# Optimization experiments

Hardware: AMD Instinct MI355X
Metric: run time of the kernel (lower is better)

The kernel has to match this reference:

```python
import jax, jax.numpy as jnp
import numpy as np

ITERS = 10
LAM = 0.1
EPS = 1e-5
DN = ('NCHW', 'OIHW', 'NCHW')


def conv2d(x, w, b, pad, dil=1):
    y = jax.lax.conv_general_dilated(
        x, w, window_strides=(1, 1), padding=((pad, pad), (pad, pad)),
        rhs_dilation=(dil, dil), dimension_numbers=DN)
    return y + b[None, :, None, None]


def avg_pool3(x):
    # F.avg_pool2d(k=3, s=1, p=1, count_include_pad=True): zero-pad then /9
    k = jnp.ones((1, 1, 3, 3), x.dtype) / 9.0
    return jax.lax.conv_general_dilated(
        x, k, window_strides=(1, 1), padding=((1, 1), (1, 1)), dimension_numbers=DN)


def setup_inputs() -> dict:
    key = jax.random.key(0)
    ks = jax.random.split(key, 16)
    B, H, W = 8, 512, 512
    G = 8  # guidance_channels
    s = 0.1
    return {
        'x': jax.random.normal(ks[0], (B, 1, H, W), jnp.float32),
        'gw1': jax.random.normal(ks[1], (16, 1, 3, 3), jnp.float32) * s,
        'gb1': jax.random.normal(ks[2], (16,), jnp.float32) * s,
        'bn_gamma': jax.random.normal(ks[3], (16,), jnp.float32) * s + 1.0,
        'bn_beta': jax.random.normal(ks[4], (16,), jnp.float32) * s,
        'bn_mean': jax.random.normal(ks[5], (16,), jnp.float32) * s,
        'bn_var': jax.random.uniform(ks[6], (16,), jnp.float32, 0.5, 1.5),
        'gw2': jax.random.normal(ks[7], (G, 16, 3, 3), jnp.float32) * s,
        'gb2': jax.random.normal(ks[8], (G,), jnp.float32) * s,
        'cw1': jax.random.normal(ks[9], (32, 4 + G, 3, 3), jnp.float32) * s,
        'cb1': jax.random.normal(ks[10], (32,), jnp.float32) * s,
        'cw2': jax.random.normal(ks[11], (16, 32, 3, 3), jnp.float32) * s,
        'cb2': jax.random.normal(ks[12], (16,), jnp.float32) * s,
        'cw3': jax.random.normal(ks[13], (4, 16, 3, 3), jnp.float32) * s,
        'cb3': jax.random.normal(ks[14], (4,), jnp.float32) * s,
    }


def reference(x, gw1, gb1, bn_gamma, bn_beta, bn_mean, bn_var, gw2, gb2,
              cw1, cb1, cw2, cb2, cw3, cb3):
    # guidance encoder on smoothed input (BN in eval mode with running stats)
    xs = avg_pool3(x)
    g = conv2d(xs, gw1, gb1, pad=2, dil=2)
    inv = bn_gamma / jnp.sqrt(bn_var + EPS)
    g = g * inv[None, :, None, None] + (bn_beta - bn_mean * inv)[None, :, None, None]
    g = jax.nn.relu(g)
    guidance = jax.lax.stop_gradient(jax.nn.sigmoid(conv2d(g, gw2, gb2, pad=1)))

    def step(x, _):
        xp = jnp.pad(x, ((0, 0), (0, 0), (1, 1), (1, 1)), mode='edge')
        gN = xp[:, :, :-2, 1:-1] - x
        gS = xp[:, :, 2:, 1:-1] - x
        gE = xp[:, :, 1:-1, 2:] - x
        gW = xp[:, :, 1:-1, :-2] - x
        comb = jnp.concatenate([gN, gS, gE, gW, guidance], axis=1)
        c = jax.nn.relu(conv2d(comb, cw1, cb1, pad=1))
        c = jax.nn.relu(conv2d(c, cw2, cb2, pad=1))
        c = jax.nn.sigmoid(conv2d(c, cw3, cb3, pad=1))
        cN, cS, cE, cWd = c[:, 0:1], c[:, 1:2], c[:, 2:3], c[:, 3:4]
        x = x + LAM * (cN * gN + cS * gS + cE * gE + cWd * gW)
        return x, None

    x, _ = jax.lax.scan(step, x, None, length=ITERS)
    return x
```

## Files before the change

### kernel.cpp

```cpp
#include <hip/hip_runtime.h>
#include <hip/hip_bf16.h>

#define HH 512
#define WW 512
#define NB 8
#define TT 16
#define BSG 384
#define BSI 256
#define EPSV 1e-5f
#define LAMV 0.1f

typedef __attribute__((ext_vector_type(4))) float f32x4;
typedef __attribute__((ext_vector_type(4))) short s16x4;
typedef __attribute__((ext_vector_type(8))) short s16x8;

#define MFMA16 __builtin_amdgcn_mfma_f32_16x16x32_bf16

#define W2PK 0
#define W3PK 9216
#define W1PKG 10816
#define W1PKU 14912
#define WPKTOT 21056

__device__ __forceinline__ float sigmoidf_(float v) { return 1.0f / (1.0f + __expf(-v)); }

__device__ __forceinline__ short f2bf(float f) {
    __hip_bfloat16 h = __float2bfloat16(f);
    short s; __builtin_memcpy(&s, &h, 2); return s;
}
__device__ __forceinline__ unsigned pack2bf(float a, float b) {
    __hip_bfloat16 ha = __float2bfloat16(a), hb = __float2bfloat16(b);
    unsigned short ua, ub;
    __builtin_memcpy(&ua, &ha, 2); __builtin_memcpy(&ub, &hb, 2);
    return (unsigned)ua | ((unsigned)ub << 16);
}

__global__ __launch_bounds__(256) void prep_kernel(
    const float* __restrict__ cw1, const float* __restrict__ cw2,
    const float* __restrict__ cw3, unsigned short* __restrict__ wpk)
{
    const int tid = threadIdx.x;
    for (int e = tid; e < 4608; e += 256) {
        int ch = e & 31, co = (e >> 5) & 15, t = e >> 9;
        wpk[W2PK / 2 + e] = (unsigned short)f2bf(cw2[(co * 32 + ch) * 9 + t]);
    }
    for (int e = tid; e < 800; e += 256) {
        int k = e % 160, row = e / 160;
        float v = 0.f;
        if (row < 4 && k < 144) { int tp = k / 16, ci = k & 15; v = cw3[(row * 16 + ci) * 9 + tp]; }
        wpk[W3PK / 2 + e] = (unsigned short)f2bf(v);
    }
    for (int e = tid; e < 2048; e += 256) {
        int k = e & 63, co = e >> 6;
        float v = 0.f;
        if (k < 36) { int tp = k >> 2, ch = k & 3; v = cw1[(co * 12 + ch) * 9 + tp]; }
        wpk[W1PKG / 2 + e] = (unsigned short)f2bf(v);
    }
    for (int e = tid; e < 3072; e += 256) {
        int k = e % 96, co = e / 96;
        float v = 0.f;
        if (k < 72) { int tp = k >> 3, ch = k & 7; v = cw1[(co * 12 + 4 + ch) * 9 + tp]; }
        wpk[W1PKU / 2 + e] = (unsigned short)f2bf(v);
    }
}

__global__ __launch_bounds__(BSG) void guidance_kernel(
    const float* __restrict__ x, const float* __restrict__ gw1, const float* __restrict__ gb1,
    const float* __restrict__ bng, const float* __restrict__ bnb, const float* __restrict__ bnm,
    const float* __restrict__ bnv, const float* __restrict__ gw2, const float* __restrict__ gb2,
    unsigned short* __restrict__ guid16)
{
    __shared__ __align__(16) float s_wg1[9][16];
    __shared__ __align__(16) float s_wg2[16][9][8];
    __shared__ float s_inv[16], s_off[16], s_b1[16], s_b2[8];
    __shared__ float s_x[24][25];
    __shared__ float s_xs[22][23];
    __shared__ float s_g[16][18][19];

    const int tid = threadIdx.x;
    const int b  = blockIdx.z;
    const int i0 = blockIdx.y * TT, j0 = blockIdx.x * TT;
    const int o = i0 - 4, p = j0 - 4;
    const float* xb = x + (size_t)b * HH * WW;

    for (int e = tid; e < 144; e += BSG) { int co = e % 16, t = e / 16; s_wg1[t][co] = gw1[co * 9 + t]; }
    for (int e = tid; e < 1152; e += BSG) {
        int co = e % 8, t = (e / 8) % 9, ci = e / 72;
        s_wg2[ci][t][co] = gw2[(co * 16 + ci) * 9 + t];
    }
    if (tid < 16) {
        float iv = bng[tid] * rsqrtf(bnv[tid] + EPSV);
        s_inv[tid] = iv; s_off[tid] = bnb[tid] - bnm[tid] * iv; s_b1[tid] = gb1[tid];
    }
    if (tid < 8) s_b2[tid] = gb2[tid];

    for (int e = tid; e < 576; e += BSG) {
        int r = e / 24, c = e % 24;
        int gi = o + r, gj = p + c;
        float v = 0.f;
        if (gi >= 0 && gi < HH && gj >= 0 && gj < WW) v = xb[gi * WW + gj];
        s_x[r][c] = v;
    }
    __syncthreads();

    for (int e = tid; e < 484; e += BSG) {
        int a = e / 22, bb = e % 22;
        int gi = o + a + 1, gj = p + bb + 1;
        float v = 0.f;
        if (gi >= 0 && gi < HH && gj >= 0 && gj < WW) {
            float s = 0.f;
            #pragma unroll
            for (int dr = 0; dr < 3; ++dr)
                #pragma unroll
                for (int dc = 0; dc < 3; ++dc) s += s_x[a + dr][bb + dc];
            v = s * (1.0f / 9.0f);
        }
        s_xs[a][bb] = v;
    }
    __syncthreads();

    for (int e = tid; e < 324; e += BSG) {
        int a = e / 18, bb = e % 18;
        int gi = o + a + 3, gj = p + bb + 3;
        bool in = (gi >= 0 && gi < HH && gj >= 0 && gj < WW);
        float acc[16];
        #pragma unroll
        for (int k = 0; k < 16; ++k) acc[k] = s_b1[k];
        #pragma unroll
        for (int kh = 0; kh < 3; ++kh)
            #pragma unroll
            for (int kw = 0; kw < 3; ++kw) {
                float av = s_xs[a + 2 * kh][bb + 2 * kw];
                #pragma unroll
                for (int q4 = 0; q4 < 4; ++q4) {
                    const float4 w = *(const float4*)&s_wg1[kh * 3 + kw][q4 * 4];
                    acc[q4*4+0] = fmaf(w.x, av, acc[q4*4+0]);
                    acc[q4*4+1] = fmaf(w.y, av, acc[q4*4+1]);
                    acc[q4*4+2] = fmaf(w.z, av, acc[q4*4+2]);
                    acc[q4*4+3] = fmaf(w.w, av, acc[q4*4+3]);
                }
            }
        #pragma unroll
        for (int k = 0; k < 16; ++k) {
            float val = acc[k] * s_inv[k] + s_off[k];
            s_g[k][a][bb] = in ? fmaxf(val, 0.f) : 0.f;
        }
    }
    __syncthreads();

    if (tid < 256) {
        int a = tid / 16, bb = tid % 16;
        int gi = i0 + a, gj = j0 + bb;
        float acc[8];
        #pragma unroll
        for (int k = 0; k < 8; ++k) acc[k] = s_b2[k];
        for (int ci = 0; ci < 16; ++ci)
            #pragma unroll
            for (int t9 = 0; t9 < 9; ++t9) {
                float av = s_g[ci][a + t9 / 3][bb + t9 % 3];
                #pragma unroll
                for (int q4 = 0; q4 < 2; ++q4) {
                    const float4 w = *(const float4*)&s_wg2[ci][t9][q4 * 4];
                    acc[q4*4+0] = fmaf(w.x, av, acc[q4*4+0]);
                    acc[q4*4+1] = fmaf(w.y, av, acc[q4*4+1]);
                    acc[q4*4+2] = fmaf(w.z, av, acc[q4*4+2]);
                    acc[q4*4+3] = fmaf(w.w, av, acc[q4*4+3]);
                }
            }
        uint4 u;
        u.x = pack2bf(sigmoidf_(acc[0]), sigmoidf_(acc[1]));
        u.y = pack2bf(sigmoidf_(acc[2]), sigmoidf_(acc[3]));
        u.z = pack2bf(sigmoidf_(acc[4]), sigmoidf_(acc[5]));
        u.w = pack2bf(sigmoidf_(acc[6]), sigmoidf_(acc[7]));
        *(uint4*)&guid16[(((size_t)b * HH + gi) * WW + gj) * 8] = u;
    }
}

__global__ __launch_bounds__(BSI) void iter_kernel(
    const float* __restrict__ xin, float* __restrict__ xout,
    const unsigned short* __restrict__ guid16,
    const unsigned short* __restrict__ wpk, const float* __restrict__ cb1,
    const float* __restrict__ cb2, const float* __restrict__ cb3)
{
    constexpr int ACTG = 2304;
    constexpr int ACTU = 6176;
    constexpr int C1   = 13920;
    constexpr int C2   = 40800;
    constexpr int C3   = C1;
    constexpr int TOT  = 51744;
    constexpr int C1P  = 6720;
    constexpr int C2P  = 5472;

    __shared__ __align__(16) char S[TOT];
    float* s_x = (float*)S;

    const int tid = threadIdx.x;
    const int bz = blockIdx.z;
    const int i0 = blockIdx.y * TT, j0 = blockIdx.x * TT;
    const int o = i0 - 4, p = j0 - 4;
    const float* xb = xin + (size_t)bz * HH * WW;

    for (int e = tid; e < 576; e += BSI) {
        int r = e / 24, c = e % 24;
        int gi = min(max(o + r, 0), HH - 1);
        int gj = min(max(p + c, 0), WW - 1);
        s_x[e] = xb[gi * WW + gj];
    }

    const int lane = tid & 63;
    const int g = lane >> 4;
    const int col = lane & 15;
    const int wv = tid >> 6;

    const float bias2_v = cb2[col];
    const float bias3_v = (col < 4) ? cb3[col] : 0.f;
    const float b1v0 = cb1[col];
    const float b1v1 = cb1[col + 16];

    s16x8 fw2[9], fw3[5], fwg[4], fwu[6];
    #pragma unroll
    for (int t = 0; t < 9; ++t)
        fw2[t] = *(const s16x8*)&wpk[W2PK / 2 + (t * 16 + col) * 32 + g * 8];
    {
        int w3r = col < 4 ? col : 4;
        #pragma unroll
        for (int q = 0; q < 5; ++q)
            fw3[q] = *(const s16x8*)&wpk[W3PK / 2 + w3r * 160 + q * 32 + g * 8];
    }
    #pragma unroll
    for (int h = 0; h < 2; ++h) {
        #pragma unroll
        for (int mf = 0; mf < 2; ++mf)
            fwg[h * 2 + mf] = *(const s16x8*)&wpk[W1PKG / 2 + (col + 16 * h) * 64 + mf * 32 + g * 8];
        #pragma unroll
        for (int q = 0; q < 3; ++q)
            fwu[h * 3 + q] = *(const s16x8*)&wpk[W1PKU / 2 + (col + 16 * h) * 96 + q * 32 + g * 8];
    }
    __syncthreads();

    for (int e = tid; e < 484; e += BSI) {
        int r = e / 22, c = e % 22;
        int gi = o + 1 + r, gj = p + 1 + c;
        bool in = ((unsigned)gi < (unsigned)HH) && ((unsigned)gj < (unsigned)WW);
        float v  = s_x[(r + 1) * 24 + c + 1];
        float gN = s_x[(r + 0) * 24 + c + 1] - v;
        float gS = s_x[(r + 2) * 24 + c + 1] - v;
        float gE = s_x[(r + 1) * 24 + c + 2] - v;
        float gW = s_x[(r + 1) * 24 + c + 0] - v;
        if (!in) { gN = gS = gE = gW = 0.f; }
        *(uint2*)&S[ACTG + (r * 22 + c) * 8] = make_uint2(pack2bf(gN, gS), pack2bf(gE, gW));
        uint4 gu = make_uint4(0u, 0u, 0u, 0u);
        if (in) gu = *(const uint4*)&guid16[(((size_t)bz * HH + gi) * WW + gj) * 8];
        *(uint4*)&S[ACTU + (r * 22 + c) * 16] = gu;
    }
    __syncthreads();

    {
        const int t0 = 2 * g, t1 = t0 + 1;
        const int dr0 = t0 / 3, dc0 = t0 % 3, dr1 = t1 / 3, dc1 = t1 % 3;
        for (int t = wv; t < 30; t += 4) {
            int band = t / 3, m3 = t % 3;
            int tc = m3 * 8 - (m3 >> 1) * 4;
            int prA = band * 2 + (col >> 3), pcA = tc + (col & 7);
            s16x4 a0 = *(const s16x4*)&S[ACTG + ((prA + dr0) * 22 + (pcA + dc0)) * 8];
            s16x4 a1 = *(const s16x4*)&S[ACTG + ((prA + dr1) * 22 + (pcA + dc1)) * 8];
            s16x4 a2 = *(const s16x4*)&S[ACTG + ((prA + 2) * 22 + (pcA + 2)) * 8];
            s16x8 A1 = __builtin_shufflevector(a0, a1, 0, 1, 2, 3, 4, 5, 6, 7);
            s16x8 A2 = __builtin_shufflevector(a2, a2, 0, 1, 2, 3, 0, 1, 2, 3);
            s16x8 Au[3];
            #pragma unroll
            for (int q = 0; q < 3; ++q) {
                int tg = q * 4 + g;
                int dtr = tg / 3, dtc = tg % 3;
                if (tg <= 8)
                    Au[q] = *(const s16x8*)&S[ACTU + ((prA + dtr) * 22 + (pcA + dtc)) * 16];
                else
                    Au[q] = (s16x8){0, 0, 0, 0, 0, 0, 0, 0};
            }
            int prD = band * 2 + (g >> 1);
            int pc0 = tc + ((4 * g) & 7);
            int giD = o + 2 + prD;
            bool rin = (unsigned)giD < (unsigned)HH;
            #pragma unroll
            for (int h = 0; h < 2; ++h) {
                int co = col + 16 * h;
                float bi = h ? b1v1 : b1v0;
                f32x4 acc = {bi, bi, bi, bi};
                acc = MFMA16(A1, fwg[h * 2 + 0], acc, 0, 0, 0);
                acc = MFMA16(A2, fwg[h * 2 + 1], acc, 0, 0, 0);
                acc = MFMA16(Au[0], fwu[h * 3 + 0], acc, 0, 0, 0);
                acc = MFMA16(Au[1], fwu[h * 3 + 1], acc, 0, 0, 0);
                acc = MFMA16(Au[2], fwu[h * 3 + 2], acc, 0, 0, 0);
                #pragma unroll
                for (int i = 0; i < 4; ++i) {
                    int pcD = pc0 + i;
                    bool in = rin && ((unsigned)(p + 2 + pcD) < (unsigned)WW);
                    float v = in ? fmaxf(acc[i], 0.f) : 0.f;
                    *(short*)&S[C1 + (co >> 3) * C1P + (prD * 21 + pcD) * 16 + (co & 7) * 2] = f2bf(v);
                }
            }
        }
    }
    __syncthreads();

    for (int t = wv; t < 27; t += 4) {
        int band = t / 3, m3 = t % 3;
        int tc = m3 * 8 - (m3 >> 1) * 6;
        int prA = band * 2 + (col >> 3), pcA = tc + (col & 7);
        f32x4 acc = {0.f, 0.f, 0.f, 0.f};
        #pragma unroll
        for (int tp = 0; tp < 9; ++tp) {
            int dr = tp / 3, dc = tp % 3;
            s16x8 Af = *(const s16x8*)&S[C1 + g * C1P + ((prA + dr) * 21 + (pcA + dc)) * 16];
            acc = MFMA16(Af, fw2[tp], acc, 0, 0, 0);
        }
        int prD = band * 2 + (g >> 1);
        int pc0 = tc + ((4 * g) & 7);
        bool rin = (unsigned)(o + 3 + prD) < (unsigned)HH;
        #pragma unroll
        for (int i = 0; i < 4; ++i) {
            int pcD = pc0 + i;
            bool in = rin && ((unsigned)(p + 3 + pcD) < (unsigned)WW);
            float v = in ? fmaxf(acc[i] + bias2_v, 0.f) : 0.f;
            *(short*)&S[C2 + (col >> 3) * C2P + (prD * 19 + pcD) * 16 + (col & 7) * 2] = f2bf(v);
        }
    }
    __syncthreads();

    for (int t = wv; t < 16; t += 4) {
        int band = t >> 1, tc = (t & 1) * 8;
        int rA = band * 2 + (col >> 3), cA = tc + (col & 7);
        f32x4 acc = {0.f, 0.f, 0.f, 0.f};
        #pragma unroll
        for (int q = 0; q < 5; ++q) {
            int tp = 2 * q + (g >> 1); if (tp > 8) tp = 8;
            int dr = tp / 3, dc = tp % 3;
            int half = g & 1;
            s16x8 Af = *(const s16x8*)&S[C2 + half * C2P + ((rA + dr) * 19 + (cA + dc)) * 16];
            acc = MFMA16(Af, fw3[q], acc, 0, 0, 0);
        }
        if (col < 4) {
            int rD = band * 2 + (g >> 1), c0 = tc + ((4 * g) & 7);
            #pragma unroll
            for (int i = 0; i < 4; ++i)
                *(float*)&S[C3 + ((rD * 16 + c0 + i) * 4 + col) * 4] = acc[i] + bias3_v;
        }
    }
    __syncthreads();

    {
        int r = tid >> 4, c = tid & 15;
        f32x4 cc = *(const f32x4*)&S[C3 + tid * 16];
        float cN = sigmoidf_(cc[0]), cS = sigmoidf_(cc[1]);
        float cE = sigmoidf_(cc[2]), cWd = sigmoidf_(cc[3]);
        float v  = s_x[(r + 4) * 24 + c + 4];
        float gN = s_x[(r + 3) * 24 + c + 4] - v;
        float gS = s_x[(r + 5) * 24 + c + 4] - v;
        float gE = s_x[(r + 4) * 24 + c + 5] - v;
        float gW = s_x[(r + 4) * 24 + c + 3] - v;
        xout[((size_t)bz * HH + (i0 + r)) * WW + (j0 + c)] =
            v + LAMV * (cN * gN + cS * gS + cE * gE + cWd * gW);
    }
}

extern "C" void kernel_launch(void* const* d_in, const int* in_sizes, int n_in,
                              void* d_out, int out_size, void* d_ws, size_t ws_size,
                              hipStream_t stream) {
    (void)in_sizes; (void)n_in; (void)out_size; (void)ws_size;
    const float* x   = (const float*)d_in[0];
    const float* gw1 = (const float*)d_in[1];
    const float* gb1 = (const float*)d_in[2];
    const float* bng = (const float*)d_in[3];
    const float* bnb = (const float*)d_in[4];
    const float* bnm = (const float*)d_in[5];
    const float* bnv = (const float*)d_in[6];
    const float* gw2 = (const float*)d_in[7];
    const float* gb2 = (const float*)d_in[8];
    const float* cw1 = (const float*)d_in[9];
    const float* cb1 = (const float*)d_in[10];
    const float* cw2 = (const float*)d_in[11];
    const float* cb2 = (const float*)d_in[12];
    const float* cw3 = (const float*)d_in[13];
    const float* cb3 = (const float*)d_in[14];
    float* out = (float*)d_out;

    char* base = (char*)d_ws;
    const size_t PX    = (size_t)NB * HH * WW;
    const size_t GU16B = PX * 8 * 2;
    const size_t XB    = PX * 4;

    unsigned short* guid16 = (unsigned short*)base;
    float* bufA            = (float*)(base + GU16B);
    unsigned short* wpk    = (unsigned short*)(base + GU16B + XB);

    dim3 grid(WW / TT, HH / TT, NB);
    prep_kernel<<<1, 256, 0, stream>>>(cw1, cw2, cw3, wpk);
    guidance_kernel<<<grid, BSG, 0, stream>>>(x, gw1, gb1, bng, bnb, bnm, bnv, gw2, gb2, guid16);

    const float* cur = x;
    for (int it = 0; it < 10; ++it) {
        float* dst = (it & 1) ? out : bufA;
        iter_kernel<<<grid, BSI, 0, stream>>>(cur, dst, guid16, wpk, cb1, cb2, cb3);
        cur = dst;
    }
}
```

Measured before the change: 1.724 ms.

## Move guidance conv2 to bf16 MFMA, shrink LDS pitches, remap iter block order

```diff
diff --git a/kernel.cpp b/kernel.cpp
--- a/kernel.cpp
+++ b/kernel.cpp
@@ -5,7 +5,6 @@
 #define WW 512
 #define NB 8
 #define TT 16
-#define BSG 384
 #define BSI 256
 #define EPSV 1e-5f
 #define LAMV 0.1f
@@ -20,7 +19,8 @@
 #define W3PK 9216
 #define W1PKG 10816
 #define W1PKU 14912
-#define WPKTOT 21056
+#define W4PK  21056
+#define WPKTOT 26176
 
 __device__ __forceinline__ float sigmoidf_(float v) { return 1.0f / (1.0f + __expf(-v)); }
 
@@ -37,7 +37,8 @@
 
 __global__ __launch_bounds__(256) void prep_kernel(
     const float* __restrict__ cw1, const float* __restrict__ cw2,
-    const float* __restrict__ cw3, unsigned short* __restrict__ wpk)
+    const float* __restrict__ cw3, const float* __restrict__ gw2,
+    unsigned short* __restrict__ wpk)
 {
     const int tid = threadIdx.x;
     for (int e = tid; e < 4608; e += 256) {
@@ -62,116 +63,138 @@
         if (k < 72) { int tp = k >> 3, ch = k & 7; v = cw1[(co * 12 + 4 + ch) * 9 + tp]; }
         wpk[W1PKU / 2 + e] = (unsigned short)f2bf(v);
     }
-}
-
-__global__ __launch_bounds__(BSG) void guidance_kernel(
+    for (int e = tid; e < 2560; e += 256) {
+        int k = e % 160, col = e / 160;
+        float v = 0.f;
+        if (col < 8 && k < 144) { int tp = k / 16, ci = k & 15; v = gw2[(col * 16 + ci) * 9 + tp]; }
+        wpk[W4PK / 2 + e] = (unsigned short)f2bf(v);
+    }
+}
+
+__global__ __launch_bounds__(256) void guidance_kernel(
     const float* __restrict__ x, const float* __restrict__ gw1, const float* __restrict__ gb1,
     const float* __restrict__ bng, const float* __restrict__ bnb, const float* __restrict__ bnm,
-    const float* __restrict__ bnv, const float* __restrict__ gw2, const float* __restrict__ gb2,
-    unsigned short* __restrict__ guid16)
+    const float* __restrict__ bnv, const float* __restrict__ gb2,
+    const unsigned short* __restrict__ wpk, unsigned short* __restrict__ guid16)
 {
-    __shared__ __align__(16) float s_wg1[9][16];
-    __shared__ __align__(16) float s_wg2[16][9][8];
-    __shared__ float s_inv[16], s_off[16], s_b1[16], s_b2[8];
-    __shared__ float s_x[24][25];
-    __shared__ float s_xs[22][23];
-    __shared__ float s_g[16][18][19];
+    constexpr int WG1 = 0, BNO = 576, SX = 768, SXS = 3904, SG = 6608, SR = 768;
+    constexpr int GP = 18 * 18 * 16;
+    __shared__ __align__(16) char S[16976];
 
     const int tid = threadIdx.x;
     const int b  = blockIdx.z;
     const int i0 = blockIdx.y * TT, j0 = blockIdx.x * TT;
-    const int o = i0 - 4, p = j0 - 4;
     const float* xb = x + (size_t)b * HH * WW;
 
-    for (int e = tid; e < 144; e += BSG) { int co = e % 16, t = e / 16; s_wg1[t][co] = gw1[co * 9 + t]; }
-    for (int e = tid; e < 1152; e += BSG) {
-        int co = e % 8, t = (e / 8) % 9, ci = e / 72;
-        s_wg2[ci][t][co] = gw2[(co * 16 + ci) * 9 + t];
+    const int lane = tid & 63;
+    const int g = lane >> 4;
+    const int col = lane & 15;
+    const int wv = tid >> 6;
+
+    for (int e = tid; e < 144; e += 256) {
+        int co = e % 16, t = e / 16;
+        ((float*)&S[WG1])[t * 16 + co] = gw1[co * 9 + t];
     }
     if (tid < 16) {
         float iv = bng[tid] * rsqrtf(bnv[tid] + EPSV);
-        s_inv[tid] = iv; s_off[tid] = bnb[tid] - bnm[tid] * iv; s_b1[tid] = gb1[tid];
-    }
-    if (tid < 8) s_b2[tid] = gb2[tid];
-
-    for (int e = tid; e < 576; e += BSG) {
-        int r = e / 24, c = e % 24;
-        int gi = o + r, gj = p + c;
-        float v = 0.f;
-        if (gi >= 0 && gi < HH && gj >= 0 && gj < WW) v = xb[gi * WW + gj];
-        s_x[r][c] = v;
-    }
-    __syncthreads();
-
-    for (int e = tid; e < 484; e += BSG) {
-        int a = e / 22, bb = e % 22;
-        int gi = o + a + 1, gj = p + bb + 1;
-        float v = 0.f;
-        if (gi >= 0 && gi < HH && gj >= 0 && gj < WW) {
+        ((float*)&S[BNO])[tid]      = iv;
+        ((float*)&S[BNO + 64])[tid] = bnb[tid] - bnm[tid] * iv;
+        ((float*)&S[BNO + 128])[tid] = gb1[tid];
+    }
+    s16x8 fw4[5];
+    #pragma unroll
+    for (int q = 0; q < 5; ++q)
+        fw4[q] = *(const s16x8*)&wpk[W4PK / 2 + col * 160 + q * 32 + g * 8];
+    const float b2v = (col < 8) ? gb2[col] : 0.f;
+
+    for (int e = tid; e < 784; e += 256) {
+        int u = e / 28, v = e % 28;
+        int gi = i0 - 6 + u, gj = j0 - 6 + v;
+        float val = 0.f;
+        if ((unsigned)gi < (unsigned)HH && (unsigned)gj < (unsigned)WW) val = xb[gi * WW + gj];
+        ((float*)&S[SX])[e] = val;
+    }
+    __syncthreads();
+
+    for (int e = tid; e < 676; e += 256) {
+        int u = e / 26, v = e % 26;
+        int gi = i0 - 5 + u, gj = j0 - 5 + v;
+        float val = 0.f;
+        if ((unsigned)gi < (unsigned)HH && (unsigned)gj < (unsigned)WW) {
             float s = 0.f;
             #pragma unroll
-            for (int dr = 0; dr < 3; ++dr)
+            for (int du = 0; du < 3; ++du)
                 #pragma unroll
-                for (int dc = 0; dc < 3; ++dc) s += s_x[a + dr][bb + dc];
-            v = s * (1.0f / 9.0f);
-        }
-        s_xs[a][bb] = v;
-    }
-    __syncthreads();
-
-    for (int e = tid; e < 324; e += BSG) {
-        int a = e / 18, bb = e % 18;
-        int gi = o + a + 3, gj = p + bb + 3;
-        bool in = (gi >= 0 && gi < HH && gj >= 0 && gj < WW);
+                for (int dv = 0; dv < 3; ++dv)
+                    s += ((float*)&S[SX])[(u + du) * 28 + (v + dv)];
+            val = s * (1.0f / 9.0f);
+        }
+        ((float*)&S[SXS])[e] = val;
+    }
+    __syncthreads();
+
+    for (int e = tid; e < 324; e += 256) {
+        int r = e / 18, c = e % 18;
+        int gi = i0 - 1 + r, gj = j0 - 1 + c;
+        bool in = (unsigned)gi < (unsigned)HH && (unsigned)gj < (unsigned)WW;
         float acc[16];
         #pragma unroll
-        for (int k = 0; k < 16; ++k) acc[k] = s_b1[k];
+        for (int k = 0; k < 16; ++k) acc[k] = ((float*)&S[BNO + 128])[k];
         #pragma unroll
         for (int kh = 0; kh < 3; ++kh)
             #pragma unroll
             for (int kw = 0; kw < 3; ++kw) {
-                float av = s_xs[a + 2 * kh][bb + 2 * kw];
+                float av = ((float*)&S[SXS])[(r + 2 * kh + 2) * 26 + (c + 2 * kw + 2)];
                 #pragma unroll
                 for (int q4 = 0; q4 < 4; ++q4) {
-                    const float4 w = *(const float4*)&s_wg1[kh * 3 + kw][q4 * 4];
+                    const float4 w = *(const float4*)&((float*)&S[WG1])[(kh * 3 + kw) * 16 + q4 * 4];
                     acc[q4*4+0] = fmaf(w.x, av, acc[q4*4+0]);
                     acc[q4*4+1] = fmaf(w.y, av, acc[q4*4+1]);
                     acc[q4*4+2] = fmaf(w.z, av, acc[q4*4+2]);
                     acc[q4*4+3] = fmaf(w.w, av, acc[q4*4+3]);
                 }
             }
+        float gval[16];
         #pragma unroll
         for (int k = 0; k < 16; ++k) {
-            float val = acc[k] * s_inv[k] + s_off[k];
-            s_g[k][a][bb] = in ? fmaxf(val, 0.f) : 0.f;
-        }
-    }
-    __syncthreads();
-
-    if (tid < 256) {
-        int a = tid / 16, bb = tid % 16;
-        int gi = i0 + a, gj = j0 + bb;
-        float acc[8];
-        #pragma unroll
-        for (int k = 0; k < 8; ++k) acc[k] = s_b2[k];
-        for (int ci = 0; ci < 16; ++ci)
-            #pragma unroll
-            for (int t9 = 0; t9 < 9; ++t9) {
-                float av = s_g[ci][a + t9 / 3][bb + t9 % 3];
-                #pragma unroll
-                for (int q4 = 0; q4 < 2; ++q4) {
-                    const float4 w = *(const float4*)&s_wg2[ci][t9][q4 * 4];
-                    acc[q4*4+0] = fmaf(w.x, av, acc[q4*4+0]);
-                    acc[q4*4+1] = fmaf(w.y, av, acc[q4*4+1]);
-                    acc[q4*4+2] = fmaf(w.z, av, acc[q4*4+2]);
-                    acc[q4*4+3] = fmaf(w.w, av, acc[q4*4+3]);
-                }
+            float v = acc[k] * ((float*)&S[BNO])[k] + ((float*)&S[BNO + 64])[k];
+            gval[k] = in ? fmaxf(v, 0.f) : 0.f;
+        }
+        uint4 h0, h1;
+        h0.x = pack2bf(gval[0], gval[1]);  h0.y = pack2bf(gval[2], gval[3]);
+        h0.z = pack2bf(gval[4], gval[5]);  h0.w = pack2bf(gval[6], gval[7]);
+        h1.x = pack2bf(gval[8], gval[9]);  h1.y = pack2bf(gval[10], gval[11]);
+        h1.z = pack2bf(gval[12], gval[13]); h1.w = pack2bf(gval[14], gval[15]);
+        *(uint4*)&S[SG + (r * 18 + c) * 16]      = h0;
+        *(uint4*)&S[SG + GP + (r * 18 + c) * 16] = h1;
+    }
+    __syncthreads();
+
+    for (int t = wv; t < 16; t += 4) {
+        int band = t >> 1, tc = (t & 1) * 8;
+        int rA = band * 2 + (col >> 3), cA = tc + (col & 7);
+        f32x4 acc = {0.f, 0.f, 0.f, 0.f};
+        #pragma unroll
+        for (int q = 0; q < 5; ++q) {
+            int tp = 2 * q + (g >> 1); if (tp > 8) tp = 8;
+            int dr = tp / 3, dc = tp % 3;
+            s16x8 Af = *(const s16x8*)&S[SG + (g & 1) * GP + ((rA + dr) * 18 + (cA + dc)) * 16];
+            acc = MFMA16(Af, fw4[q], acc, 0, 0, 0);
+        }
+        if (col < 8) {
+            int rD = band * 2 + (g >> 1), c0 = tc + ((4 * g) & 7);
+            #pragma unroll
+            for (int i = 0; i < 4; ++i) {
+                float s = sigmoidf_(acc[i] + b2v);
+                *(short*)&S[SR + ((rD * 16 + c0 + i) * 8 + col) * 2] = f2bf(s);
             }
-        uint4 u;
-        u.x = pack2bf(sigmoidf_(acc[0]), sigmoidf_(acc[1]));
-        u.y = pack2bf(sigmoidf_(acc[2]), sigmoidf_(acc[3]));
-        u.z = pack2bf(sigmoidf_(acc[4]), sigmoidf_(acc[5]));
-        u.w = pack2bf(sigmoidf_(acc[6]), sigmoidf_(acc[7]));
+        }
+    }
+    __syncthreads();
+
+    {
+        uint4 u = *(const uint4*)&S[SR + tid * 16];
+        int gi = i0 + (tid >> 4), gj = j0 + (tid & 15);
         *(uint4*)&guid16[(((size_t)b * HH + gi) * WW + gj) * 8] = u;
     }
 }
@@ -185,18 +208,21 @@
     constexpr int ACTG = 2304;
     constexpr int ACTU = 6176;
     constexpr int C1   = 13920;
-    constexpr int C2   = 40800;
+    constexpr int C2   = 39520;
     constexpr int C3   = C1;
-    constexpr int TOT  = 51744;
-    constexpr int C1P  = 6720;
-    constexpr int C2P  = 5472;
+    constexpr int TOT  = 49888;
+    constexpr int C1P  = 6400;
+    constexpr int C2P  = 5184;
 
     __shared__ __align__(16) char S[TOT];
     float* s_x = (float*)S;
 
     const int tid = threadIdx.x;
-    const int bz = blockIdx.z;
-    const int i0 = blockIdx.y * TT, j0 = blockIdx.x * TT;
+    const int flat = blockIdx.x;
+    const int nid  = (flat & 7) * 1024 + (flat >> 3);
+    const int bz   = nid >> 10;
+    const int i0   = ((nid >> 5) & 31) * TT;
+    const int j0   = (nid & 31) * TT;
     const int o = i0 - 4, p = j0 - 4;
     const float* xb = xin + (size_t)bz * HH * WW;
 
@@ -205,6 +231,14 @@
         int gi = min(max(o + r, 0), HH - 1);
         int gj = min(max(p + c, 0), WW - 1);
         s_x[e] = xb[gi * WW + gj];
+    }
+    for (int e = tid; e < 484; e += BSI) {
+        int r = e / 22, c = e % 22;
+        int gi = o + 1 + r, gj = p + 1 + c;
+        bool in = ((unsigned)gi < (unsigned)HH) && ((unsigned)gj < (unsigned)WW);
+        uint4 gu = make_uint4(0u, 0u, 0u, 0u);
+        if (in) gu = *(const uint4*)&guid16[(((size_t)bz * HH + gi) * WW + gj) * 8];
+        *(uint4*)&S[ACTU + (r * 22 + c) * 16] = gu;
     }
 
     const int lane = tid & 63;
@@ -249,9 +283,6 @@
         float gW = s_x[(r + 1) * 24 + c + 0] - v;
         if (!in) { gN = gS = gE = gW = 0.f; }
         *(uint2*)&S[ACTG + (r * 22 + c) * 8] = make_uint2(pack2bf(gN, gS), pack2bf(gE, gW));
-        uint4 gu = make_uint4(0u, 0u, 0u, 0u);
-        if (in) gu = *(const uint4*)&guid16[(((size_t)bz * HH + gi) * WW + gj) * 8];
-        *(uint4*)&S[ACTU + (r * 22 + c) * 16] = gu;
     }
     __syncthreads();
 
@@ -296,7 +327,7 @@
                     int pcD = pc0 + i;
                     bool in = rin && ((unsigned)(p + 2 + pcD) < (unsigned)WW);
                     float v = in ? fmaxf(acc[i], 0.f) : 0.f;
-                    *(short*)&S[C1 + (co >> 3) * C1P + (prD * 21 + pcD) * 16 + (co & 7) * 2] = f2bf(v);
+                    *(short*)&S[C1 + (co >> 3) * C1P + (prD * 20 + pcD) * 16 + (co & 7) * 2] = f2bf(v);
                 }
             }
         }
@@ -311,7 +342,7 @@
         #pragma unroll
         for (int tp = 0; tp < 9; ++tp) {
             int dr = tp / 3, dc = tp % 3;
-            s16x8 Af = *(const s16x8*)&S[C1 + g * C1P + ((prA + dr) * 21 + (pcA + dc)) * 16];
+            s16x8 Af = *(const s16x8*)&S[C1 + g * C1P + ((prA + dr) * 20 + (pcA + dc)) * 16];
             acc = MFMA16(Af, fw2[tp], acc, 0, 0, 0);
         }
         int prD = band * 2 + (g >> 1);
@@ -322,7 +353,7 @@
             int pcD = pc0 + i;
             bool in = rin && ((unsigned)(p + 3 + pcD) < (unsigned)WW);
             float v = in ? fmaxf(acc[i] + bias2_v, 0.f) : 0.f;
-            *(short*)&S[C2 + (col >> 3) * C2P + (prD * 19 + pcD) * 16 + (col & 7) * 2] = f2bf(v);
+            *(short*)&S[C2 + (col >> 3) * C2P + (prD * 18 + pcD) * 16 + (col & 7) * 2] = f2bf(v);
         }
     }
     __syncthreads();
@@ -336,7 +367,7 @@
             int tp = 2 * q + (g >> 1); if (tp > 8) tp = 8;
             int dr = tp / 3, dc = tp % 3;
             int half = g & 1;
-            s16x8 Af = *(const s16x8*)&S[C2 + half * C2P + ((rA + dr) * 19 + (cA + dc)) * 16];
+            s16x8 Af = *(const s16x8*)&S[C2 + half * C2P + ((rA + dr) * 18 + (cA + dc)) * 16];
             acc = MFMA16(Af, fw3[q], acc, 0, 0, 0);
         }
         if (col < 4) {
@@ -393,14 +424,14 @@
     float* bufA            = (float*)(base + GU16B);
     unsigned short* wpk    = (unsigned short*)(base + GU16B + XB);
 
-    dim3 grid(WW / TT, HH / TT, NB);
-    prep_kernel<<<1, 256, 0, stream>>>(cw1, cw2, cw3, wpk);
-    guidance_kernel<<<grid, BSG, 0, stream>>>(x, gw1, gb1, bng, bnb, bnm, bnv, gw2, gb2, guid16);
+    dim3 grid3(WW / TT, HH / TT, NB);
+    prep_kernel<<<1, 256, 0, stream>>>(cw1, cw2, cw3, gw2, wpk);
+    guidance_kernel<<<grid3, 256, 0, stream>>>(x, gw1, gb1, bng, bnb, bnm, bnv, gb2, wpk, guid16);
 
     const float* cur = x;
     for (int it = 0; it < 10; ++it) {
         float* dst = (it & 1) ? out : bufA;
-        iter_kernel<<<grid, BSI, 0, stream>>>(cur, dst, guid16, wpk, cb1, cb2, cb3);
+        iter_kernel<<<8192, BSI, 0, stream>>>(cur, dst, guid16, wpk, cb1, cb2, cb3);
         cur = dst;
     }
 }
```

Result: faster. 1.510 ms (-12.4%).
